# Kernel tuning notes

Hardware: AMD Instinct MI355X
Metric: run time of the kernel (lower is better)

Reference implementation:

```python
import jax, jax.numpy as jnp
import numpy as np

B, N, C = 8, 4096, 256
HEADS, SR = 8, 4
LN_EPS = 1e-5

def setup_inputs() -> dict:
    key = jax.random.key(0)
    ks = jax.random.split(key, 8)
    std = 0.02
    x = jax.random.normal(ks[0], (B, N, C), dtype=jnp.float32)
    q_w = jax.random.normal(ks[1], (C, C), dtype=jnp.float32) * std          # [in,out]
    kv_w = jax.random.normal(ks[2], (C, 2 * C), dtype=jnp.float32) * std     # [in,2*out]
    fan_out = SR * SR * C
    sr_w = jax.random.normal(ks[3], (C, C, SR, SR), dtype=jnp.float32) * np.sqrt(2.0 / fan_out)  # OIHW
    sr_b = jnp.zeros((C,), dtype=jnp.float32)
    ln_w = jnp.ones((C,), dtype=jnp.float32)
    ln_b = jnp.zeros((C,), dtype=jnp.float32)
    proj_w = jax.random.normal(ks[4], (C, C), dtype=jnp.float32) * std
    proj_b = jnp.zeros((C,), dtype=jnp.float32)
    return {"x": x, "H": 64, "W": 64, "q_w": q_w, "kv_w": kv_w, "sr_w": sr_w,
            "sr_b": sr_b, "ln_w": ln_w, "ln_b": ln_b, "proj_w": proj_w, "proj_b": proj_b}


def reference(x, H, W, q_w, kv_w, sr_w, sr_b, ln_w, ln_b, proj_w, proj_b):
    Bb, Nn, Cc = x.shape
    hd = Cc // HEADS
    scale = hd ** -0.5
    # q: [B, heads, N, hd]
    q = (x @ q_w).reshape(Bb, Nn, HEADS, hd).transpose(0, 2, 1, 3)
    # spatial reduction: conv(stride=sr) + LayerNorm
    x_ = x.transpose(0, 2, 1).reshape(Bb, Cc, H, W)
    x_ = jax.lax.conv_general_dilated(
        x_, sr_w, window_strides=(SR, SR), padding="VALID",
        dimension_numbers=("NCHW", "OIHW", "NCHW")) + sr_b[None, :, None, None]
    x_ = x_.reshape(Bb, Cc, -1).transpose(0, 2, 1)  # [B, Nk, C]
    mu = x_.mean(-1, keepdims=True)
    var = x_.var(-1, keepdims=True)
    x_ = (x_ - mu) * jax.lax.rsqrt(var + LN_EPS) * ln_w + ln_b
    # kv: [B, Nk, 2, heads, hd]
    Nk = x_.shape[1]
    kv = (x_ @ kv_w).reshape(Bb, Nk, 2, HEADS, hd)
    k = kv[:, :, 0].transpose(0, 2, 1, 3)  # [B, heads, Nk, hd]
    v = kv[:, :, 1].transpose(0, 2, 1, 3)  # [B, heads, Nk, hd]
    attn = jnp.einsum("bhnd,bhmd->bhnm", q, k) * scale
    attn = jax.nn.softmax(attn, axis=-1)
    out = jnp.einsum("bhnm,bhmd->bhnd", attn, v)  # [B, heads, N, hd]
    out = out.transpose(0, 2, 1, 3).reshape(Bb, Nn, Cc)
    return out @ proj_w + proj_b
```

## Files before the change

kernel.cpp:

```cpp
#include <hip/hip_runtime.h>
#include <hip/hip_bf16.h>
#include <math.h>

#define DI __device__ __forceinline__

static constexpr float SCALE = 0.17677669529663687f;

typedef short bf16x8 __attribute__((ext_vector_type(8)));
typedef float f32x4 __attribute__((ext_vector_type(4)));

__device__ int   g_isf32;
__device__ unsigned short g_qwh[256 * 256],  g_qwl[256 * 256];
__device__ unsigned short g_kvwh[512 * 256], g_kvwl[512 * 256];
__device__ unsigned short g_pwh[256 * 256],  g_pwl[256 * 256];
__device__ unsigned short g_wth[(size_t)256 * 4096];
__device__ unsigned short g_wtl[(size_t)256 * 4096];
__device__ unsigned short g_q[(size_t)64 * 4096 * 32];
__device__ unsigned short g_k[(size_t)64 * 256 * 32];
__device__ unsigned short g_vt[(size_t)64 * 32 * 256];
__device__ float g_convp[(size_t)16 * 2048 * 256];
__device__ unsigned short g_lnh[2048 * 256], g_lnl[2048 * 256];
__device__ unsigned short g_attnb[(size_t)32768 * 256];

DI float bfbits2f(unsigned short b) { return __uint_as_float(((unsigned)b) << 16); }

DI unsigned short f2bf(float f) {
  unsigned u = __float_as_uint(f);
  unsigned r = (u + 0x7fffu + ((u >> 16) & 1u)) >> 16;
  return (unsigned short)r;
}

DI float4 ld_bf4(const unsigned short* p) {
  ushort4 u = *(const ushort4*)p;
  return make_float4(bfbits2f(u.x), bfbits2f(u.y), bfbits2f(u.z), bfbits2f(u.w));
}

DI float ld1(const void* p, size_t i, int f32) {
  return f32 ? ((const float*)p)[i] : bfbits2f(((const unsigned short*)p)[i]);
}

DI float4 ld4(const void* p, size_t i, int f32) {
  if (f32) return *(const float4*)((const float*)p + i);
  return ld_bf4((const unsigned short*)p + i);
}

__global__ void k_detect(const void* __restrict__ xp) {
  __shared__ float red[256];
  int t = threadIdx.x;
  const unsigned short* p = (const unsigned short*)xp;
  float m = 0.f;
  for (int i = t; i < 16384; i += 256) {
    float v = fabsf(bfbits2f(p[i]));
    m = (v == v && v < 1e30f) ? fmaxf(m, v) : 1e30f;
  }
  red[t] = m;
  __syncthreads();
  for (int s = 128; s > 0; s >>= 1) {
    if (t < s) red[t] = fmaxf(red[t], red[t + s]);
    __syncthreads();
  }
  if (t == 0) g_isf32 = (red[0] > 1e4f) ? 1 : 0;
}

__global__ void k_prep(const void* __restrict__ qw, const void* __restrict__ kvw,
                       const void* __restrict__ pwp, const void* __restrict__ srw) {
  const int f32 = g_isf32;
  int bid = blockIdx.x;
  if (bid < 1024) {
    int e = bid * 256 + threadIdx.x;
    float v;
    unsigned short *dh, *dl;
    size_t di;
    if (e < 65536) {
      int o = e >> 8, c = e & 255;
      v = ld1(qw, (size_t)c * 256 + o, f32) * SCALE;
      dh = g_qwh; dl = g_qwl; di = e;
    } else if (e < 196608) {
      int e2 = e - 65536;
      int o = e2 >> 8, c = e2 & 255;
      v = ld1(kvw, (size_t)c * 512 + o, f32);
      dh = g_kvwh; dl = g_kvwl; di = e2;
    } else {
      int e2 = e - 196608;
      int o = e2 >> 8, c = e2 & 255;
      v = ld1(pwp, (size_t)c * 256 + o, f32);
      dh = g_pwh; dl = g_pwl; di = e2;
    }
    unsigned short hi = f2bf(v);
    dh[di] = hi;
    dl[di] = f2bf(v - bfbits2f(hi));
  } else {
    int e = (bid - 1024) * 256 + threadIdx.x;
    int o = e >> 12, kk = e & 4095;
    int tap = kk >> 8, ci = kk & 255;
    float v = ld1(srw, (size_t)o * 4096 + ci * 16 + tap, f32);
    unsigned short hi = f2bf(v);
    g_wth[e] = hi;
    g_wtl[e] = f2bf(v - bfbits2f(hi));
  }
}

template <int MODE>
__launch_bounds__(256, 3)
__global__ void k_mgemm(const void* __restrict__ Ax,
                        const void* __restrict__ biasp, void* __restrict__ outp) {
  constexpr bool XIN = (MODE == 0 || MODE == 1);
  constexpr bool AH  = (MODE != 3);

  __shared__ __align__(16) short sa_h[64 * 40];
  __shared__ __align__(16) short sa_l[64 * 40];
  __shared__ __align__(16) short sb_h[256 * 40];
  __shared__ __align__(16) short sb_l[256 * 40];

  const int f32 = g_isf32;
  const int tid = threadIdx.x;
  const int m0 = blockIdx.x * 64;
  const int nblk = (MODE == 2) ? blockIdx.y : 0;
  const int kz = (MODE == 1) ? blockIdx.z * 256 : 0;
  const int wave = tid >> 6, lane = tid & 63;
  const int quad = lane >> 4, l15 = lane & 15;

  f32x4 acc[4][4] = {};

  for (int it = 0; it < 8; ++it) {
    const int kb = kz + it * 32;
    {
      int row = tid >> 2, chunk = tid & 3;
      size_t src;
      if constexpr (MODE == 1) {
        int m = m0 + row;
        int bb = m >> 8, sp = m & 255;
        int oh = sp >> 4, ow = sp & 15;
        int tap = kb >> 8, kh = tap >> 2, kw = tap & 3;
        int n = (4 * oh + kh) * 64 + 4 * ow + kw;
        src = (((size_t)(bb * 4096 + n)) << 8) + (kb & 255) + chunk * 8;
      } else {
        src = (((size_t)(m0 + row)) << 8) + kb + chunk * 8;
      }
      if constexpr (XIN) {
        float4 v0 = ld4(Ax, src, f32);
        float4 v1 = ld4(Ax, src + 4, f32);
        ushort4 h0, l0, h1, l1;
        h0.x = f2bf(v0.x); l0.x = f2bf(v0.x - bfbits2f(h0.x));
        h0.y = f2bf(v0.y); l0.y = f2bf(v0.y - bfbits2f(h0.y));
        h0.z = f2bf(v0.z); l0.z = f2bf(v0.z - bfbits2f(h0.z));
        h0.w = f2bf(v0.w); l0.w = f2bf(v0.w - bfbits2f(h0.w));
        h1.x = f2bf(v1.x); l1.x = f2bf(v1.x - bfbits2f(h1.x));
        h1.y = f2bf(v1.y); l1.y = f2bf(v1.y - bfbits2f(h1.y));
        h1.z = f2bf(v1.z); l1.z = f2bf(v1.z - bfbits2f(h1.z));
        h1.w = f2bf(v1.w); l1.w = f2bf(v1.w - bfbits2f(h1.w));
        *(ushort4*)&sa_h[row * 40 + chunk * 8]     = h0;
        *(ushort4*)&sa_h[row * 40 + chunk * 8 + 4] = h1;
        *(ushort4*)&sa_l[row * 40 + chunk * 8]     = l0;
        *(ushort4*)&sa_l[row * 40 + chunk * 8 + 4] = l1;
      } else if constexpr (MODE == 2) {
        *(uint4*)&sa_h[row * 40 + chunk * 8] = *(const uint4*)&g_lnh[src];
        *(uint4*)&sa_l[row * 40 + chunk * 8] = *(const uint4*)&g_lnl[src];
      } else {
        *(uint4*)&sa_h[row * 40 + chunk * 8] = *(const uint4*)&g_attnb[src];
      }
    }
    {
      constexpr int BKROW = (MODE == 1) ? 4096 : 256;
      const unsigned short* Bh = (MODE == 0) ? g_qwh : (MODE == 1) ? g_wth
                               : (MODE == 2) ? g_kvwh : g_pwh;
      const unsigned short* Bl = (MODE == 0) ? g_qwl : (MODE == 1) ? g_wtl
                               : (MODE == 2) ? g_kvwl : g_pwl;
#pragma unroll
      for (int i = 0; i < 4; ++i) {
        int linear = tid + 256 * i;
        int row = linear >> 2, chunk = linear & 3;
        size_t src = (size_t)(nblk * 256 + row) * BKROW + kb + chunk * 8;
        *(uint4*)&sb_h[row * 40 + chunk * 8] = *(const uint4*)&Bh[src];
        *(uint4*)&sb_l[row * 40 + chunk * 8] = *(const uint4*)&Bl[src];
      }
    }
    __syncthreads();
#pragma unroll
    for (int mt = 0; mt < 4; ++mt) {
      bf16x8 a_h = *(const bf16x8*)&sa_h[(mt * 16 + l15) * 40 + quad * 8];
      bf16x8 a_l;
      if constexpr (AH) a_l = *(const bf16x8*)&sa_l[(mt * 16 + l15) * 40 + quad * 8];
#pragma unroll
      for (int j = 0; j < 4; ++j) {
        int nrow = (4 * wave + j) * 16 + l15;
        bf16x8 b_h = *(const bf16x8*)&sb_h[nrow * 40 + quad * 8];
        bf16x8 b_l = *(const bf16x8*)&sb_l[nrow * 40 + quad * 8];
        f32x4 c = acc[mt][j];
        c = __builtin_amdgcn_mfma_f32_16x16x32_bf16(a_h, b_h, c, 0, 0, 0);
        if constexpr (AH)
          c = __builtin_amdgcn_mfma_f32_16x16x32_bf16(a_l, b_h, c, 0, 0, 0);
        c = __builtin_amdgcn_mfma_f32_16x16x32_bf16(a_h, b_l, c, 0, 0, 0);
        acc[mt][j] = c;
      }
    }
    __syncthreads();
  }

#pragma unroll
  for (int mt = 0; mt < 4; ++mt) {
#pragma unroll
    for (int j = 0; j < 4; ++j) {
#pragma unroll
      for (int r = 0; r < 4; ++r) {
        int m = m0 + mt * 16 + quad * 4 + r;
        int c = nblk * 256 + (4 * wave + j) * 16 + l15;
        float v = acc[mt][j][r];
        if constexpr (MODE == 0) {
          int b = m >> 12, n = m & 4095;
          int h = c >> 5, d = c & 31;
          g_q[(((size_t)(b * 8 + h) * 4096 + n) << 5) + d] = f2bf(v);
        } else if constexpr (MODE == 1) {
          g_convp[((size_t)blockIdx.z * 2048 + m) * 256 + c] = v;
        } else if constexpr (MODE == 2) {
          int s = c >> 8, h = (c >> 5) & 7, d = c & 31;
          int bb = m >> 8, nk = m & 255;
          if (s == 0)
            g_k[(((size_t)(bb * 8 + h) * 256 + nk) << 5) + d] = f2bf(v);
          else
            g_vt[(((size_t)(bb * 8 + h) * 32 + d) << 8) + nk] = f2bf(v);
        } else {
          float rr = v + ld1(biasp, c, f32);
          if (f32) ((float*)outp)[(size_t)m * 256 + c] = rr;
          else     ((unsigned short*)outp)[(size_t)m * 256 + c] = f2bf(rr);
        }
      }
    }
  }
}

__global__ void k_redln(const void* __restrict__ srb,
                        const void* __restrict__ lw, const void* __restrict__ lb) {
  const int f32 = g_isf32;
  int row = blockIdx.x, t = threadIdx.x;
  size_t idx = (size_t)row * 256 + t;
  float v = 0.f;
#pragma unroll
  for (int z = 0; z < 16; ++z) v += g_convp[(size_t)z * (2048 * 256) + idx];
  v += ld1(srb, t, f32);
  float s = v, sq = v * v;
#pragma unroll
  for (int off = 32; off >= 1; off >>= 1) {
    s += __shfl_down(s, off, 64);
    sq += __shfl_down(sq, off, 64);
  }
  __shared__ float rs[4], rq[4];
  int wid = t >> 6;
  if ((t & 63) == 0) { rs[wid] = s; rq[wid] = sq; }
  __syncthreads();
  float st = rs[0] + rs[1] + rs[2] + rs[3];
  float qt = rq[0] + rq[1] + rq[2] + rq[3];
  float mu = st * (1.0f / 256.0f);
  float var = qt * (1.0f / 256.0f) - mu * mu;
  float r = rsqrtf(var + 1e-5f);
  float o = (v - mu) * r * ld1(lw, t, f32) + ld1(lb, t, f32);
  unsigned short hi = f2bf(o);
  g_lnh[idx] = hi;
  g_lnl[idx] = f2bf(o - bfbits2f(hi));
}

__launch_bounds__(256, 3)
__global__ void k_attn() {
  __shared__ short smem[18688];
  short* sk  = smem;
  short* svt = smem + 10240;

  const int tid = threadIdx.x;
  const int bh = blockIdx.y;
  const int b = bh >> 3, h = bh & 7;

  {
    const uint4* gk = (const uint4*)(g_k + (size_t)bh * 8192);
    const uint4* gv = (const uint4*)(g_vt + (size_t)bh * 8192);
    for (int i = tid; i < 1024; i += 256) {
      int key = i >> 2, part = i & 3;
      *(uint4*)&sk[key * 40 + part * 8] = gk[i];
      int d = i >> 5, off = (i & 31) * 8;
      *(uint4*)&svt[d * 264 + off] = gv[i];
    }
  }
  __syncthreads();

  const int wave = tid >> 6, lane = tid & 63;
  const int quad = lane >> 4, l15 = lane & 15;
  const int n0 = blockIdx.x * 64 + wave * 16;

  bf16x8 qv = *(const bf16x8*)(g_q + ((size_t)bh * 4096 + n0 + l15) * 32 + quad * 8);

  f32x4 sacc[16];
#pragma unroll
  for (int t = 0; t < 16; ++t) {
    bf16x8 kf = *(const bf16x8*)&sk[(t * 16 + l15) * 40 + quad * 8];
    f32x4 c = {0.f, 0.f, 0.f, 0.f};
    sacc[t] = __builtin_amdgcn_mfma_f32_16x16x32_bf16(kf, qv, c, 0, 0, 0);
  }

  float m = sacc[0][0];
#pragma unroll
  for (int t = 0; t < 16; ++t) {
#pragma unroll
    for (int r = 0; r < 4; ++r) m = fmaxf(m, sacc[t][r]);
  }
  m = fmaxf(m, __shfl_xor(m, 16, 64));
  m = fmaxf(m, __shfl_xor(m, 32, 64));

  unsigned plo[16], phi[16];
  float ls = 0.f;
#pragma unroll
  for (int t = 0; t < 16; ++t) {
    unsigned short p0 = f2bf(__expf(sacc[t][0] - m));
    unsigned short p1 = f2bf(__expf(sacc[t][1] - m));
    unsigned short p2 = f2bf(__expf(sacc[t][2] - m));
    unsigned short p3 = f2bf(__expf(sacc[t][3] - m));
    ls += bfbits2f(p0) + bfbits2f(p1) + bfbits2f(p2) + bfbits2f(p3);
    plo[t] = (unsigned)p0 | ((unsigned)p1 << 16);
    phi[t] = (unsigned)p2 | ((unsigned)p3 << 16);
  }
  ls += __shfl_xor(ls, 16, 64);
  ls += __shfl_xor(ls, 32, 64);
  float inv = 1.0f / ls;

  f32x4 o0 = {0.f, 0.f, 0.f, 0.f}, o1 = {0.f, 0.f, 0.f, 0.f};
  const int laneA = ((quad & 1) << 5) + l15;
  const int laneB = laneA + 16;
  const bool hiT = quad >= 2;
#pragma unroll
  for (int c = 0; c < 8; ++c) {
    unsigned a0 = __shfl(plo[2 * c], laneA, 64), b0 = __shfl(plo[2 * c + 1], laneA, 64);
    unsigned a1 = __shfl(phi[2 * c], laneA, 64), b1 = __shfl(phi[2 * c + 1], laneA, 64);
    unsigned a2 = __shfl(plo[2 * c], laneB, 64), b2 = __shfl(plo[2 * c + 1], laneB, 64);
    unsigned a3 = __shfl(phi[2 * c], laneB, 64), b3 = __shfl(phi[2 * c + 1], laneB, 64);
    uint4 pk = make_uint4(hiT ? b0 : a0, hiT ? b1 : a1, hiT ? b2 : a2, hiT ? b3 : a3);
    bf16x8 pf = *(bf16x8*)&pk;
    bf16x8 v0 = *(const bf16x8*)&svt[l15 * 264 + c * 32 + quad * 8];
    bf16x8 v1 = *(const bf16x8*)&svt[(16 + l15) * 264 + c * 32 + quad * 8];
    o0 = __builtin_amdgcn_mfma_f32_16x16x32_bf16(v0, pf, o0, 0, 0, 0);
    o1 = __builtin_amdgcn_mfma_f32_16x16x32_bf16(v1, pf, o1, 0, 0, 0);
  }

  size_t base = ((size_t)(b * 4096 + n0 + l15)) * 256 + h * 32 + quad * 4;
  ushort4 u0, u1;
  u0.x = f2bf(o0[0] * inv); u0.y = f2bf(o0[1] * inv);
  u0.z = f2bf(o0[2] * inv); u0.w = f2bf(o0[3] * inv);
  u1.x = f2bf(o1[0] * inv); u1.y = f2bf(o1[1] * inv);
  u1.z = f2bf(o1[2] * inv); u1.w = f2bf(o1[3] * inv);
  *(ushort4*)&g_attnb[base]      = u0;
  *(ushort4*)&g_attnb[base + 16] = u1;
}

extern "C" void kernel_launch(void* const* d_in, const int* in_sizes, int n_in,
                              void* d_out, int out_size, void* d_ws, size_t ws_size,
                              hipStream_t stream) {
  const void* x   = d_in[0];
  const void* qw  = d_in[3];
  const void* kvw = d_in[4];
  const void* srw = d_in[5];
  const void* srb = d_in[6];
  const void* lnw = d_in[7];
  const void* lnb = d_in[8];
  const void* pw  = d_in[9];
  const void* pb  = d_in[10];

  k_detect<<<1, 256, 0, stream>>>(x);
  k_prep<<<5120, 256, 0, stream>>>(qw, kvw, pw, srw);
  k_mgemm<0><<<dim3(512, 1), 256, 0, stream>>>(x, nullptr, nullptr);
  k_mgemm<1><<<dim3(32, 1, 16), 256, 0, stream>>>(x, nullptr, nullptr);
  k_redln<<<2048, 256, 0, stream>>>(srb, lnw, lnb);
  k_mgemm<2><<<dim3(32, 2), 256, 0, stream>>>(nullptr, nullptr, nullptr);
  k_attn<<<dim3(64, 64), 256, 0, stream>>>();
  k_mgemm<3><<<dim3(512, 1), 256, 0, stream>>>(nullptr, pb, d_out);
}
```

Before: 241.2 us.

## Inline dtype detection per kernel, store conv partials in bf16, raise attn occupancy

Removes the separate single-block detection kernel and instead has each kernel detect the input dtype inline by scanning 32 words of x. It also stores the split-K conv partial sums as bf16 instead of fp32, which halves the traffic of the partial-sum write and the reduction read. The attention kernel's launch bounds rise from 3 to 4 blocks per CU. In exchange, rounding the partial sums to bf16 loses precision before the LayerNorm, and detecting the dtype from only 32 words is a weaker heuristic than the full scan.

```diff
diff --git a/kernel.cpp b/kernel.cpp
--- a/kernel.cpp
+++ b/kernel.cpp
@@ -9,7 +9,6 @@
 typedef short bf16x8 __attribute__((ext_vector_type(8)));
 typedef float f32x4 __attribute__((ext_vector_type(4)));
 
-__device__ int   g_isf32;
 __device__ unsigned short g_qwh[256 * 256],  g_qwl[256 * 256];
 __device__ unsigned short g_kvwh[512 * 256], g_kvwl[512 * 256];
 __device__ unsigned short g_pwh[256 * 256],  g_pwl[256 * 256];
@@ -18,7 +17,7 @@
 __device__ unsigned short g_q[(size_t)64 * 4096 * 32];
 __device__ unsigned short g_k[(size_t)64 * 256 * 32];
 __device__ unsigned short g_vt[(size_t)64 * 32 * 256];
-__device__ float g_convp[(size_t)16 * 2048 * 256];
+__device__ unsigned short g_convp[(size_t)16 * 2048 * 256];
 __device__ unsigned short g_lnh[2048 * 256], g_lnl[2048 * 256];
 __device__ unsigned short g_attnb[(size_t)32768 * 256];
 
@@ -44,27 +43,24 @@
   return ld_bf4((const unsigned short*)p + i);
 }
 
-__global__ void k_detect(const void* __restrict__ xp) {
-  __shared__ float red[256];
-  int t = threadIdx.x;
-  const unsigned short* p = (const unsigned short*)xp;
-  float m = 0.f;
-  for (int i = t; i < 16384; i += 256) {
-    float v = fabsf(bfbits2f(p[i]));
-    m = (v == v && v < 1e30f) ? fmaxf(m, v) : 1e30f;
-  }
-  red[t] = m;
-  __syncthreads();
-  for (int s = 128; s > 0; s >>= 1) {
-    if (t < s) red[t] = fmaxf(red[t], red[t + s]);
-    __syncthreads();
-  }
-  if (t == 0) g_isf32 = (red[0] > 1e4f) ? 1 : 0;
+DI int detect_f32(const void* xp) {
+  const unsigned* p = (const unsigned*)xp;
+  unsigned m0 = 0, m1 = 0;
+#pragma unroll
+  for (int i = 0; i < 32; ++i) {
+    unsigned w = p[i];
+    unsigned lo = w & 0x7fffu, hi = (w >> 16) & 0x7fffu;
+    m0 = lo > m0 ? lo : m0;
+    m1 = hi > m1 ? hi : m1;
+  }
+  unsigned mm = m0 > m1 ? m0 : m1;
+  return mm >= 0x4680u ? 1 : 0;
 }
 
 __global__ void k_prep(const void* __restrict__ qw, const void* __restrict__ kvw,
-                       const void* __restrict__ pwp, const void* __restrict__ srw) {
-  const int f32 = g_isf32;
+                       const void* __restrict__ pwp, const void* __restrict__ srw,
+                       const void* __restrict__ xp) {
+  const int f32 = detect_f32(xp);
   int bid = blockIdx.x;
   if (bid < 1024) {
     int e = bid * 256 + threadIdx.x;
@@ -106,19 +102,27 @@
                         const void* __restrict__ biasp, void* __restrict__ outp) {
   constexpr bool XIN = (MODE == 0 || MODE == 1);
   constexpr bool AH  = (MODE != 3);
+  constexpr int BKROW = (MODE == 1) ? 4096 : 256;
 
   __shared__ __align__(16) short sa_h[64 * 40];
   __shared__ __align__(16) short sa_l[64 * 40];
   __shared__ __align__(16) short sb_h[256 * 40];
   __shared__ __align__(16) short sb_l[256 * 40];
 
-  const int f32 = g_isf32;
+  int f32 = 0;
+  if constexpr (XIN || MODE == 3) f32 = detect_f32(Ax);
+
   const int tid = threadIdx.x;
   const int m0 = blockIdx.x * 64;
   const int nblk = (MODE == 2) ? blockIdx.y : 0;
   const int kz = (MODE == 1) ? blockIdx.z * 256 : 0;
   const int wave = tid >> 6, lane = tid & 63;
   const int quad = lane >> 4, l15 = lane & 15;
+
+  const unsigned short* Bh = (MODE == 0) ? g_qwh : (MODE == 1) ? g_wth
+                           : (MODE == 2) ? g_kvwh : g_pwh;
+  const unsigned short* Bl = (MODE == 0) ? g_qwl : (MODE == 1) ? g_wtl
+                           : (MODE == 2) ? g_kvwl : g_pwl;
 
   f32x4 acc[4][4] = {};
 
@@ -161,18 +165,13 @@
       }
     }
     {
-      constexpr int BKROW = (MODE == 1) ? 4096 : 256;
-      const unsigned short* Bh = (MODE == 0) ? g_qwh : (MODE == 1) ? g_wth
-                               : (MODE == 2) ? g_kvwh : g_pwh;
-      const unsigned short* Bl = (MODE == 0) ? g_qwl : (MODE == 1) ? g_wtl
-                               : (MODE == 2) ? g_kvwl : g_pwl;
 #pragma unroll
       for (int i = 0; i < 4; ++i) {
-        int linear = tid + 256 * i;
-        int row = linear >> 2, chunk = linear & 3;
-        size_t src = (size_t)(nblk * 256 + row) * BKROW + kb + chunk * 8;
-        *(uint4*)&sb_h[row * 40 + chunk * 8] = *(const uint4*)&Bh[src];
-        *(uint4*)&sb_l[row * 40 + chunk * 8] = *(const uint4*)&Bl[src];
+        int lin = tid + 256 * i;
+        int row = lin >> 2, chk = lin & 3;
+        size_t src = (size_t)(nblk * 256 + row) * BKROW + kb + chk * 8;
+        *(uint4*)&sb_h[row * 40 + chk * 8] = *(const uint4*)&Bh[src];
+        *(uint4*)&sb_l[row * 40 + chk * 8] = *(const uint4*)&Bl[src];
       }
     }
     __syncthreads();
@@ -183,9 +182,9 @@
       if constexpr (AH) a_l = *(const bf16x8*)&sa_l[(mt * 16 + l15) * 40 + quad * 8];
 #pragma unroll
       for (int j = 0; j < 4; ++j) {
-        int nrow = (4 * wave + j) * 16 + l15;
-        bf16x8 b_h = *(const bf16x8*)&sb_h[nrow * 40 + quad * 8];
-        bf16x8 b_l = *(const bf16x8*)&sb_l[nrow * 40 + quad * 8];
+        int nr = (4 * wave + j) * 16 + l15;
+        bf16x8 b_h = *(const bf16x8*)&sb_h[nr * 40 + quad * 8];
+        bf16x8 b_l = *(const bf16x8*)&sb_l[nr * 40 + quad * 8];
         f32x4 c = acc[mt][j];
         c = __builtin_amdgcn_mfma_f32_16x16x32_bf16(a_h, b_h, c, 0, 0, 0);
         if constexpr (AH)
@@ -197,6 +196,7 @@
     __syncthreads();
   }
 
+  const int f32o = f32;
 #pragma unroll
   for (int mt = 0; mt < 4; ++mt) {
 #pragma unroll
@@ -211,7 +211,7 @@
           int h = c >> 5, d = c & 31;
           g_q[(((size_t)(b * 8 + h) * 4096 + n) << 5) + d] = f2bf(v);
         } else if constexpr (MODE == 1) {
-          g_convp[((size_t)blockIdx.z * 2048 + m) * 256 + c] = v;
+          g_convp[((size_t)blockIdx.z * 2048 + m) * 256 + c] = f2bf(v);
         } else if constexpr (MODE == 2) {
           int s = c >> 8, h = (c >> 5) & 7, d = c & 31;
           int bb = m >> 8, nk = m & 255;
@@ -220,23 +220,23 @@
           else
             g_vt[(((size_t)(bb * 8 + h) * 32 + d) << 8) + nk] = f2bf(v);
         } else {
-          float rr = v + ld1(biasp, c, f32);
-          if (f32) ((float*)outp)[(size_t)m * 256 + c] = rr;
-          else     ((unsigned short*)outp)[(size_t)m * 256 + c] = f2bf(rr);
+          float rr = v + ld1(biasp, c, f32o);
+          if (f32o) ((float*)outp)[(size_t)m * 256 + c] = rr;
+          else      ((unsigned short*)outp)[(size_t)m * 256 + c] = f2bf(rr);
         }
       }
     }
   }
 }
 
-__global__ void k_redln(const void* __restrict__ srb,
+__global__ void k_redln(const void* __restrict__ xp, const void* __restrict__ srb,
                         const void* __restrict__ lw, const void* __restrict__ lb) {
-  const int f32 = g_isf32;
+  const int f32 = detect_f32(xp);
   int row = blockIdx.x, t = threadIdx.x;
   size_t idx = (size_t)row * 256 + t;
   float v = 0.f;
 #pragma unroll
-  for (int z = 0; z < 16; ++z) v += g_convp[(size_t)z * (2048 * 256) + idx];
+  for (int z = 0; z < 16; ++z) v += bfbits2f(g_convp[(size_t)z * (2048 * 256) + idx]);
   v += ld1(srb, t, f32);
   float s = v, sq = v * v;
 #pragma unroll
@@ -259,7 +259,7 @@
   g_lnl[idx] = f2bf(o - bfbits2f(hi));
 }
 
-__launch_bounds__(256, 3)
+__launch_bounds__(256, 4)
 __global__ void k_attn() {
   __shared__ short smem[18688];
   short* sk  = smem;
@@ -361,12 +361,11 @@
   const void* pw  = d_in[9];
   const void* pb  = d_in[10];
 
-  k_detect<<<1, 256, 0, stream>>>(x);
-  k_prep<<<5120, 256, 0, stream>>>(qw, kvw, pw, srw);
+  k_prep<<<5120, 256, 0, stream>>>(qw, kvw, pw, srw, x);
   k_mgemm<0><<<dim3(512, 1), 256, 0, stream>>>(x, nullptr, nullptr);
   k_mgemm<1><<<dim3(32, 1, 16), 256, 0, stream>>>(x, nullptr, nullptr);
-  k_redln<<<2048, 256, 0, stream>>>(srb, lnw, lnb);
+  k_redln<<<2048, 256, 0, stream>>>(x, srb, lnw, lnb);
   k_mgemm<2><<<dim3(32, 2), 256, 0, stream>>>(nullptr, nullptr, nullptr);
   k_attn<<<dim3(64, 64), 256, 0, stream>>>();
-  k_mgemm<3><<<dim3(512, 1), 256, 0, stream>>>(nullptr, pb, d_out);
-}
+  k_mgemm<3><<<dim3(512, 1), 256, 0, stream>>>(x, pb, d_out);
+}
```

Result: faster. 235.3 us (-2.4%).
